# Optimization experiments

Measured on AMD Instinct MI355X. Metric: run time of the kernel, lower is better.

Reference implementation:

```python
import jax, jax.numpy as jnp
import numpy as np

B, S, D, H = 2, 2048, 1024, 16
HD = D // H  # head_dim = 64

def setup_inputs() -> dict:
    key = jax.random.key(0)
    ks = jax.random.split(key, 12)
    sc = 0.02
    return {
        "x": jax.random.normal(ks[0], (B, S, D), dtype=jnp.float32),
        "docking_scores": jax.random.uniform(ks[1], (B, S), dtype=jnp.float32),
        # weights stored as (in, out): y = x @ W + b (equivalent to torch Linear with W=weight.T)
        "Wq": jax.random.normal(ks[2], (D, D), dtype=jnp.float32) * sc,
        "bq": jnp.zeros((D,), dtype=jnp.float32),
        "Wk": jax.random.normal(ks[3], (D, D), dtype=jnp.float32) * sc,
        "bk": jnp.zeros((D,), dtype=jnp.float32),
        "Wv": jax.random.normal(ks[4], (D, D), dtype=jnp.float32) * sc,
        "bv": jnp.zeros((D,), dtype=jnp.float32),
        "Wo": jax.random.normal(ks[5], (D, D), dtype=jnp.float32) * sc,
        "bo": jnp.zeros((D,), dtype=jnp.float32),
        "beta": jnp.asarray(0.5, dtype=jnp.float32),
    }

def reference(x, docking_scores, Wq, bq, Wk, bk, Wv, bv, Wo, bo, beta):
    b, s, d = x.shape
    # project and split heads: (B, H, S, HD)
    def heads(y):
        return y.reshape(b, s, H, HD).transpose(0, 2, 1, 3)
    Q = heads(x @ Wq + bq)
    K = heads(x @ Wk + bk)
    V = heads(x @ Wv + bv)
    # full attention scores (B, H, S, S) — materialized as in the source
    scores = jnp.einsum('bhqd,bhkd->bhqk', Q, K) / np.float32(np.sqrt(HD))
    attn = jax.nn.softmax(scores, axis=-1)
    # docking blend: daa_type != ALL -> blend with per-key docking scores
    ds = docking_scores[:, None, None, :]  # (B, 1, 1, S)
    attn = (1.0 - beta) * attn + beta * ds
    ctx = jnp.einsum('bhqk,bhkd->bhqd', attn, V)
    ctx = ctx.transpose(0, 2, 1, 3).reshape(b, s, d)
    return ctx @ Wo + bo
```

## Files before the change

### kernel.cpp

```cpp
#include <hip/hip_runtime.h>

typedef __attribute__((ext_vector_type(8))) short short8;
typedef __attribute__((ext_vector_type(4))) short short4v;
typedef __attribute__((ext_vector_type(4))) float f32x4;

#if __has_builtin(__builtin_amdgcn_exp2f)
#define EXP2F(x) __builtin_amdgcn_exp2f(x)
#define QSCALE 0.1803368801111601f
#else
#define EXP2F(x) __expf(x)
#define QSCALE 0.125f
#endif

__device__ __forceinline__ short f2bf(float f) {
  unsigned u = __builtin_bit_cast(unsigned, f);
  u += 0x7fffu + ((u >> 16) & 1u);
  return (short)(u >> 16);
}
__device__ __forceinline__ float bf2f(short s) {
  unsigned u = ((unsigned)(unsigned short)s) << 16;
  return __builtin_bit_cast(float, u);
}
__device__ __forceinline__ void async_load16(const short* g, short* l) {
  __builtin_amdgcn_global_load_lds(
      (const __attribute__((address_space(1))) unsigned int*)g,
      (__attribute__((address_space(3))) unsigned int*)l, 16, 0, 0);
}

__global__ __launch_bounds__(256) void convert_x(const float* __restrict__ x,
                                                 short* __restrict__ xb) {
  int i = (blockIdx.x * 256 + threadIdx.x) * 4;
  float4 v = *(const float4*)(x + i);
  short4v o;
  o[0] = f2bf(v.x); o[1] = f2bf(v.y); o[2] = f2bf(v.z); o[3] = f2bf(v.w);
  *(short4v*)(xb + i) = o;
}

__global__ __launch_bounds__(256) void transpose_w(
    const float* __restrict__ W0, const float* __restrict__ W1,
    const float* __restrict__ W2, const float* __restrict__ W3,
    short* __restrict__ T0, short* __restrict__ T1,
    short* __restrict__ T2, short* __restrict__ T3) {
  const float* W; short* T;
  switch (blockIdx.z) {
    case 0: W = W0; T = T0; break;
    case 1: W = W1; T = T1; break;
    case 2: W = W2; T = T2; break;
    default: W = W3; T = T3; break;
  }
  __shared__ float tile[32][33];
  int tx = threadIdx.x & 31, ty = threadIdx.x >> 5;
  int c = blockIdx.x * 32 + tx;
  #pragma unroll
  for (int i = 0; i < 4; ++i) {
    int r = blockIdx.y * 32 + ty + i * 8;
    tile[ty + i * 8][tx] = W[(size_t)r * 1024 + c];
  }
  __syncthreads();
  int k = blockIdx.y * 32 + tx;
  #pragma unroll
  for (int i = 0; i < 4; ++i) {
    int n = blockIdx.x * 32 + ty + i * 8;
    T[(size_t)n * 1024 + k] = f2bf(tile[tx][ty + i * 8]);
  }
}

__device__ __forceinline__ void gemm_core_128(
    const short* __restrict__ A, const short* __restrict__ Bt,
    int m0, int n0, short* As, short* Bs, f32x4 acc[4][4]) {
  const int tid = threadIdx.x;
  const int wave = tid >> 6, lane = tid & 63;
  const int wm = wave >> 1, wn = wave & 1;
  const int lr = lane & 15, quad = lane >> 4;
  for (int k0 = 0; k0 < 1024; k0 += 32) {
    __syncthreads();
    #pragma unroll
    for (int c2 = 0; c2 < 2; ++c2) {
      int c = wave * 2 + c2;
      int row = c * 16 + (lane >> 2);
      int cbp = lane & 3;
      int sw = (cbp ^ ((row >> 1) & 3)) << 3;
      async_load16(A + (size_t)(m0 + row) * 1024 + k0 + sw, As + c * 512);
      async_load16(Bt + (size_t)(n0 + row) * 1024 + k0 + sw, Bs + c * 512);
    }
    __syncthreads();
    short8 af[4], bfr[4];
    #pragma unroll
    for (int i = 0; i < 4; ++i) {
      int ra = wm * 64 + i * 16 + lr;
      af[i] = *(const short8*)(As + ra * 32 + ((quad ^ ((ra >> 1) & 3)) << 3));
      int rb = wn * 64 + i * 16 + lr;
      bfr[i] = *(const short8*)(Bs + rb * 32 + ((quad ^ ((rb >> 1) & 3)) << 3));
    }
    #pragma unroll
    for (int i = 0; i < 4; ++i)
      #pragma unroll
      for (int j = 0; j < 4; ++j)
        acc[i][j] = __builtin_amdgcn_mfma_f32_16x16x32_bf16(af[i], bfr[j], acc[i][j], 0, 0, 0);
  }
}

__global__ __launch_bounds__(256, 2) void qkv_gemm(
    const short* __restrict__ xb,
    const short* __restrict__ WqT, const short* __restrict__ WkT, const short* __restrict__ WvT,
    const float* __restrict__ bq, const float* __restrict__ bk, const float* __restrict__ bv,
    short* __restrict__ Qb, short* __restrict__ Kb, short* __restrict__ Vt) {
  __shared__ short As[128 * 32];
  __shared__ short Bs[128 * 32];
  int which = blockIdx.x >> 3;
  int n0 = (blockIdx.x & 7) * 128;
  int m0 = blockIdx.y * 128;
  const short* Bt = (which == 0) ? WqT : (which == 1) ? WkT : WvT;
  const float* bias = (which == 0) ? bq : (which == 1) ? bk : bv;
  f32x4 acc[4][4] = {};
  gemm_core_128(xb, Bt, m0, n0, As, Bs, acc);
  const int lane = threadIdx.x & 63, wave = threadIdx.x >> 6;
  const int wm = wave >> 1, wn = wave & 1;
  const int lr = lane & 15, quad = lane >> 4;
  if (which < 2) {
    short* Out = (which == 0) ? Qb : Kb;
    const float scale = (which == 0) ? QSCALE : 1.0f;
    #pragma unroll
    for (int i = 0; i < 4; ++i)
      #pragma unroll
      for (int j = 0; j < 4; ++j) {
        int col = n0 + wn * 64 + j * 16 + lr;
        float bb = bias[col];
        int rowb = m0 + wm * 64 + i * 16 + quad * 4;
        #pragma unroll
        for (int r = 0; r < 4; ++r)
          Out[(size_t)(rowb + r) * 1024 + col] = f2bf((acc[i][j][r] + bb) * scale);
      }
  } else {
    #pragma unroll
    for (int i = 0; i < 4; ++i)
      #pragma unroll
      for (int j = 0; j < 4; ++j) {
        int col = n0 + wn * 64 + j * 16 + lr;
        float bb = bias[col];
        int h = col >> 6, d = col & 63;
        int rowb = m0 + wm * 64 + i * 16 + quad * 4;
        int b = rowb >> 11, s = rowb & 2047;
        short4v pk;
        #pragma unroll
        for (int r = 0; r < 4; ++r) pk[r] = f2bf(acc[i][j][r] + bb);
        *(short4v*)(Vt + ((size_t)(b * 16 + h) * 64 + d) * 2048 + s) = pk;
      }
  }
}

__global__ __launch_bounds__(256) void dsv_kernel(const short* __restrict__ Vt,
                                                  const float* __restrict__ ds,
                                                  float* __restrict__ dsV) {
  int bh = blockIdx.x, sc = blockIdx.y;
  int b = bh >> 4;
  int d = threadIdx.x >> 2, part = threadIdx.x & 3;
  const short* vrow = Vt + ((size_t)bh * 64 + d) * 2048 + sc * 256 + part * 64;
  const float* dsrow = ds + (size_t)b * 2048 + sc * 256 + part * 64;
  float acc = 0.f;
  #pragma unroll
  for (int i = 0; i < 64; i += 8) {
    short8 v = *(const short8*)(vrow + i);
    float4 f0 = *(const float4*)(dsrow + i);
    float4 f1 = *(const float4*)(dsrow + i + 4);
    acc += f0.x * bf2f(v[0]) + f0.y * bf2f(v[1]) + f0.z * bf2f(v[2]) + f0.w * bf2f(v[3]);
    acc += f1.x * bf2f(v[4]) + f1.y * bf2f(v[5]) + f1.z * bf2f(v[6]) + f1.w * bf2f(v[7]);
  }
  acc += __shfl_xor(acc, 1);
  acc += __shfl_xor(acc, 2);
  if (part == 0) atomicAdd(dsV + bh * 64 + d, acc);
}

__global__ __launch_bounds__(512, 4) void attn_kernel(
    const short* __restrict__ Qb, const short* __restrict__ Kb,
    const short* __restrict__ Vt, const float* __restrict__ dsV,
    const float* __restrict__ beta_p, short* __restrict__ ctx) {
  __shared__ short smem[32768];
  const int tid = threadIdx.x, wave = tid >> 6, lane = tid & 63;
  const int bh = blockIdx.x >> 4, qt = blockIdx.x & 15;
  const int b = bh >> 4, h = bh & 15;
  const size_t bS = (size_t)b * 2048;
  const int lr = lane & 15, quad = lane >> 4;
  const int half = wave >> 2;
  const int qg = wave & 3;
  const int q0 = qt * 128 + qg * 32;

  short* Ksh = smem + half * 8192;
  short* Vsh = Ksh + 4096;
  short* myP = smem + 16384 + wave * 2048;

  short8 qf[2][2];
  #pragma unroll
  for (int mb = 0; mb < 2; ++mb)
    #pragma unroll
    for (int c = 0; c < 2; ++c)
      qf[mb][c] = *(const short8*)(Qb + (bS + q0 + mb * 16 + lr) * 1024 + h * 64 + c * 32 + quad * 8);

  f32x4 O[2][4] = {};
  float lacc[2] = {0.f, 0.f};
  const int xs = (lr & 7) << 1;

  for (int t = 0; t < 16; ++t) {
    const int k0 = (half * 16 + t) * 64;
    __syncthreads();
    #pragma unroll
    for (int c4 = 0; c4 < 4; ++c4) {
      int c = qg * 4 + c4;
      int rloc = lane >> 3;
      int cbp = lane & 7;
      if (c < 8) {
        int rk = c * 8 + rloc;
        int sw = (cbp ^ (rk & 7)) << 3;
        async_load16(Kb + (bS + k0 + rk) * 1024 + h * 64 + sw, Ksh + c * 512);
      } else {
        int cv = c - 8;
        int rk = cv * 8 + rloc;
        int sw = (cbp ^ (rk & 7)) << 3;
        async_load16(Vt + ((size_t)bh * 64 + rk) * 2048 + k0 + sw, Vsh + cv * 512);
      }
    }
    __syncthreads();

    #pragma unroll
    for (int kb = 0; kb < 4; ++kb) {
      int krow = kb * 16 + lr;
      const short* kr = Ksh + krow * 64;
      short8 kf0 = *(const short8*)(kr + ((quad ^ (krow & 7)) << 3));
      short8 kf1 = *(const short8*)(kr + (((4 + quad) ^ (krow & 7)) << 3));
      #pragma unroll
      for (int mb = 0; mb < 2; ++mb) {
        f32x4 st = {0.f, 0.f, 0.f, 0.f};
        st = __builtin_amdgcn_mfma_f32_16x16x32_bf16(kf0, qf[mb][0], st, 0, 0, 0);
        st = __builtin_amdgcn_mfma_f32_16x16x32_bf16(kf1, qf[mb][1], st, 0, 0, 0);
        float p0 = EXP2F(st[0]), p1 = EXP2F(st[1]);
        float p2 = EXP2F(st[2]), p3 = EXP2F(st[3]);
        lacc[mb] += (p0 + p1) + (p2 + p3);
        unsigned a0 = __builtin_bit_cast(unsigned, p0) + 0x8000u;
        unsigned a1 = __builtin_bit_cast(unsigned, p1) + 0x8000u;
        unsigned a2 = __builtin_bit_cast(unsigned, p2) + 0x8000u;
        unsigned a3 = __builtin_bit_cast(unsigned, p3) + 0x8000u;
        uint2 pk;
        pk.x = (a0 >> 16) | (a1 & 0xffff0000u);
        pk.y = (a2 >> 16) | (a3 & 0xffff0000u);
        int qrl = mb * 16 + lr;
        int phys4 = (kb * 4 + quad) ^ xs;
        *(uint2*)(myP + qrl * 64 + (phys4 << 2)) = pk;
      }
    }
    #pragma unroll
    for (int kc = 0; kc < 2; ++kc) {
      short8 pf[2];
      #pragma unroll
      for (int mb = 0; mb < 2; ++mb) {
        int qrl = mb * 16 + lr;
        int phys = ((kc * 4 + quad) << 1) ^ xs;
        pf[mb] = *(const short8*)(myP + qrl * 64 + (phys << 2));
      }
      #pragma unroll
      for (int db = 0; db < 4; ++db) {
        int drow = db * 16 + lr;
        short8 vf = *(const short8*)(Vsh + drow * 64 + (((kc * 4 + quad) ^ (drow & 7)) << 3));
        #pragma unroll
        for (int mb = 0; mb < 2; ++mb)
          O[mb][db] = __builtin_amdgcn_mfma_f32_16x16x32_bf16(vf, pf[mb], O[mb][db], 0, 0, 0);
      }
    }
  }

  float* Obuf = (float*)smem;
  float* lbuf = (float*)(smem + 16384);
  __syncthreads();
  if (half == 1) {
    #pragma unroll
    for (int mb = 0; mb < 2; ++mb) {
      #pragma unroll
      for (int db = 0; db < 4; ++db)
        *(f32x4*)(Obuf + ((qg * 2 + mb) * 4 + db) * 256 + lr * 16 + quad * 4) = O[mb][db];
      lbuf[(qg * 2 + mb) * 64 + quad * 16 + lr] = lacc[mb];
    }
  }
  __syncthreads();
  if (half == 0) {
    #pragma unroll
    for (int mb = 0; mb < 2; ++mb) {
      #pragma unroll
      for (int db = 0; db < 4; ++db)
        O[mb][db] += *(const f32x4*)(Obuf + ((qg * 2 + mb) * 4 + db) * 256 + lr * 16 + quad * 4);
      lacc[mb] += lbuf[(qg * 2 + mb) * 64 + quad * 16 + lr];
      float v = lacc[mb];
      v += __shfl_xor(v, 16);
      v += __shfl_xor(v, 32);
      lacc[mb] = v;
    }
    float beta = *beta_p;
    #pragma unroll
    for (int mb = 0; mb < 2; ++mb) {
      float linv = (1.f - beta) / lacc[mb];
      #pragma unroll
      for (int db = 0; db < 4; ++db) {
        float4 dv = *(const float4*)(dsV + bh * 64 + db * 16 + quad * 4);
        short4v o;
        o[0] = f2bf(O[mb][db][0] * linv + beta * dv.x);
        o[1] = f2bf(O[mb][db][1] * linv + beta * dv.y);
        o[2] = f2bf(O[mb][db][2] * linv + beta * dv.z);
        o[3] = f2bf(O[mb][db][3] * linv + beta * dv.w);
        *(short4v*)(ctx + (bS + q0 + mb * 16 + lr) * 1024 + h * 64 + db * 16 + quad * 4) = o;
      }
    }
  }
}

__global__ __launch_bounds__(256, 2) void out_gemm(
    const short* __restrict__ ctx, const short* __restrict__ WoT,
    const float* __restrict__ bo, float* __restrict__ out) {
  __shared__ short As[64 * 32];
  __shared__ short Bs[128 * 32];
  const int n0 = blockIdx.x * 128, m0 = blockIdx.y * 64;
  const int tid = threadIdx.x, wave = tid >> 6, lane = tid & 63;
  const int wm = wave >> 1, wn = wave & 1;
  const int lr = lane & 15, quad = lane >> 4;
  f32x4 acc[2][4] = {};
  for (int k0 = 0; k0 < 1024; k0 += 32) {
    __syncthreads();
    #pragma unroll
    for (int c3 = 0; c3 < 3; ++c3) {
      int idx = wave * 3 + c3;
      int rloc = lane >> 2;
      int cbp = lane & 3;
      if (idx < 4) {
        int row = idx * 16 + rloc;
        int sw = (cbp ^ ((row >> 1) & 3)) << 3;
        async_load16(ctx + (size_t)(m0 + row) * 1024 + k0 + sw, As + idx * 512);
      } else {
        int c = idx - 4;
        int row = c * 16 + rloc;
        int sw = (cbp ^ ((row >> 1) & 3)) << 3;
        async_load16(WoT + (size_t)(n0 + row) * 1024 + k0 + sw, Bs + c * 512);
      }
    }
    __syncthreads();
    short8 af[2], bfr[4];
    #pragma unroll
    for (int i = 0; i < 2; ++i) {
      int ra = wm * 32 + i * 16 + lr;
      af[i] = *(const short8*)(As + ra * 32 + ((quad ^ ((ra >> 1) & 3)) << 3));
    }
    #pragma unroll
    for (int j = 0; j < 4; ++j) {
      int rb = wn * 64 + j * 16 + lr;
      bfr[j] = *(const short8*)(Bs + rb * 32 + ((quad ^ ((rb >> 1) & 3)) << 3));
    }
    #pragma unroll
    for (int i = 0; i < 2; ++i)
      #pragma unroll
      for (int j = 0; j < 4; ++j)
        acc[i][j] = __builtin_amdgcn_mfma_f32_16x16x32_bf16(af[i], bfr[j], acc[i][j], 0, 0, 0);
  }
  #pragma unroll
  for (int i = 0; i < 2; ++i)
    #pragma unroll
    for (int j = 0; j < 4; ++j) {
      int col = n0 + wn * 64 + j * 16 + lr;
      float bb = bo[col];
      int rowb = m0 + wm * 32 + i * 16 + quad * 4;
      #pragma unroll
      for (int r = 0; r < 4; ++r)
        out[(size_t)(rowb + r) * 1024 + col] = acc[i][j][r] + bb;
    }
}

extern "C" void kernel_launch(void* const* d_in, const int* in_sizes, int n_in,
                              void* d_out, int out_size, void* d_ws, size_t ws_size,
                              hipStream_t stream) {
  const float* x    = (const float*)d_in[0];
  const float* dsc  = (const float*)d_in[1];
  const float* Wq   = (const float*)d_in[2];
  const float* bq   = (const float*)d_in[3];
  const float* Wk   = (const float*)d_in[4];
  const float* bk   = (const float*)d_in[5];
  const float* Wv   = (const float*)d_in[6];
  const float* bv   = (const float*)d_in[7];
  const float* Wo   = (const float*)d_in[8];
  const float* bo   = (const float*)d_in[9];
  const float* beta = (const float*)d_in[10];

  char* ws = (char*)d_ws;
  const size_t MB = 1u << 20;
  short* xb  = (short*)(ws + 0 * MB);
  short* WqT = (short*)(ws + 8 * MB);
  short* WkT = (short*)(ws + 10 * MB);
  short* WvT = (short*)(ws + 12 * MB);
  short* WoT = (short*)(ws + 14 * MB);
  short* Qb  = (short*)(ws + 16 * MB);
  short* Kb  = (short*)(ws + 24 * MB);
  short* Vt  = (short*)(ws + 32 * MB);
  float* dsV = (float*)(ws + 40 * MB);
  short* ctx = xb;

  convert_x<<<4096, 256, 0, stream>>>(x, xb);
  transpose_w<<<dim3(32, 32, 4), 256, 0, stream>>>(Wq, Wk, Wv, Wo, WqT, WkT, WvT, WoT);
  qkv_gemm<<<dim3(24, 32), 256, 0, stream>>>(xb, WqT, WkT, WvT, bq, bk, bv, Qb, Kb, Vt);
  hipMemsetAsync(dsV, 0, 32 * 64 * sizeof(float), stream);
  dsv_kernel<<<dim3(32, 8), 256, 0, stream>>>(Vt, dsc, dsV);
  attn_kernel<<<512, 512, 0, stream>>>(Qb, Kb, Vt, dsV, beta, ctx);
  out_gemm<<<dim3(8, 64), 256, 0, stream>>>(ctx, WoT, bo, (float*)d_out);
}
```

Before: 213.0 us.

## Halve attention block waves, give each wave 64 query rows for K/V reuse

The attention kernel now launches 256 threads (4 waves) per block instead of 512, and each wave handles 64 query rows (4 MFMA row blocks) instead of 32. Each K/V fragment read from LDS therefore feeds twice as many MFMAs. The loader is split so one wave group loads K and the other loads V. Bf16 packing now uses v_perm, and the final reduction buffer uses a rotated column index to reduce bank conflicts. The cost is more registers per wave (accumulators double) and less latency hiding from fewer waves per block.

```diff
diff --git a/kernel.cpp b/kernel.cpp
--- a/kernel.cpp
+++ b/kernel.cpp
@@ -171,7 +171,7 @@
   if (part == 0) atomicAdd(dsV + bh * 64 + d, acc);
 }
 
-__global__ __launch_bounds__(512, 4) void attn_kernel(
+__global__ __launch_bounds__(256, 2) void attn_kernel(
     const short* __restrict__ Qb, const short* __restrict__ Kb,
     const short* __restrict__ Vt, const float* __restrict__ dsV,
     const float* __restrict__ beta_p, short* __restrict__ ctx) {
@@ -181,54 +181,53 @@
   const int b = bh >> 4, h = bh & 15;
   const size_t bS = (size_t)b * 2048;
   const int lr = lane & 15, quad = lane >> 4;
-  const int half = wave >> 2;
-  const int qg = wave & 3;
-  const int q0 = qt * 128 + qg * 32;
+  const int qg = wave & 1, half = wave >> 1;
+  const int q0 = qt * 128 + qg * 64;
+  const int lm7 = lane & 7;
+  const int l7 = lr & 7;
 
   short* Ksh = smem + half * 8192;
   short* Vsh = Ksh + 4096;
-  short* myP = smem + 16384 + wave * 2048;
-
-  short8 qf[2][2];
+  short* myP = smem + 16384 + wave * 4096;
+
+  short8 qf[4][2];
   #pragma unroll
-  for (int mb = 0; mb < 2; ++mb)
+  for (int mb = 0; mb < 4; ++mb)
     #pragma unroll
     for (int c = 0; c < 2; ++c)
       qf[mb][c] = *(const short8*)(Qb + (bS + q0 + mb * 16 + lr) * 1024 + h * 64 + c * 32 + quad * 8);
 
-  f32x4 O[2][4] = {};
-  float lacc[2] = {0.f, 0.f};
-  const int xs = (lr & 7) << 1;
+  f32x4 O[4][4] = {};
+  float lacc[4] = {0.f, 0.f, 0.f, 0.f};
+
+  const int srow = lane >> 3;
+  const int scb = (lane & 7) ^ srow;
 
   for (int t = 0; t < 16; ++t) {
     const int k0 = (half * 16 + t) * 64;
     __syncthreads();
-    #pragma unroll
-    for (int c4 = 0; c4 < 4; ++c4) {
-      int c = qg * 4 + c4;
-      int rloc = lane >> 3;
-      int cbp = lane & 7;
-      if (c < 8) {
-        int rk = c * 8 + rloc;
-        int sw = (cbp ^ (rk & 7)) << 3;
-        async_load16(Kb + (bS + k0 + rk) * 1024 + h * 64 + sw, Ksh + c * 512);
-      } else {
-        int cv = c - 8;
-        int rk = cv * 8 + rloc;
-        int sw = (cbp ^ (rk & 7)) << 3;
-        async_load16(Vt + ((size_t)bh * 64 + rk) * 2048 + k0 + sw, Vsh + cv * 512);
+    if (qg == 0) {
+      #pragma unroll
+      for (int c = 0; c < 8; ++c) {
+        int rk = c * 8 + srow;
+        async_load16(Kb + (bS + k0 + rk) * 1024 + h * 64 + scb * 8, Ksh + c * 512);
+      }
+    } else {
+      #pragma unroll
+      for (int c = 0; c < 8; ++c) {
+        int rv = c * 8 + srow;
+        async_load16(Vt + ((size_t)bh * 64 + rv) * 2048 + k0 + scb * 8, Vsh + c * 512);
       }
     }
     __syncthreads();
 
     #pragma unroll
     for (int kb = 0; kb < 4; ++kb) {
-      int krow = kb * 16 + lr;
-      const short* kr = Ksh + krow * 64;
-      short8 kf0 = *(const short8*)(kr + ((quad ^ (krow & 7)) << 3));
-      short8 kf1 = *(const short8*)(kr + (((4 + quad) ^ (krow & 7)) << 3));
-      #pragma unroll
-      for (int mb = 0; mb < 2; ++mb) {
+      const short* kr = Ksh + (kb * 16 + lr) * 64;
+      short8 kf0 = *(const short8*)(kr + ((quad ^ l7) << 3));
+      short8 kf1 = *(const short8*)(kr + (((4 + quad) ^ l7) << 3));
+      #pragma unroll
+      for (int mb = 0; mb < 4; ++mb) {
         f32x4 st = {0.f, 0.f, 0.f, 0.f};
         st = __builtin_amdgcn_mfma_f32_16x16x32_bf16(kf0, qf[mb][0], st, 0, 0, 0);
         st = __builtin_amdgcn_mfma_f32_16x16x32_bf16(kf1, qf[mb][1], st, 0, 0, 0);
@@ -240,28 +239,26 @@
         unsigned a2 = __builtin_bit_cast(unsigned, p2) + 0x8000u;
         unsigned a3 = __builtin_bit_cast(unsigned, p3) + 0x8000u;
         uint2 pk;
-        pk.x = (a0 >> 16) | (a1 & 0xffff0000u);
-        pk.y = (a2 >> 16) | (a3 & 0xffff0000u);
-        int qrl = mb * 16 + lr;
-        int phys4 = (kb * 4 + quad) ^ xs;
-        *(uint2*)(myP + qrl * 64 + (phys4 << 2)) = pk;
+        pk.x = __builtin_amdgcn_perm(a1, a0, 0x07060302u);
+        pk.y = __builtin_amdgcn_perm(a3, a2, 0x07060302u);
+        int phys = (4 * kb + quad) ^ (2 * l7);
+        *(uint2*)(myP + (mb * 16 + lr) * 64 + phys * 4) = pk;
       }
     }
     #pragma unroll
     for (int kc = 0; kc < 2; ++kc) {
-      short8 pf[2];
-      #pragma unroll
-      for (int mb = 0; mb < 2; ++mb) {
-        int qrl = mb * 16 + lr;
-        int phys = ((kc * 4 + quad) << 1) ^ xs;
-        pf[mb] = *(const short8*)(myP + qrl * 64 + (phys << 2));
+      short8 pf[4];
+      #pragma unroll
+      for (int mb = 0; mb < 4; ++mb) {
+        int phys = (8 * kc + 2 * quad) ^ (2 * l7);
+        pf[mb] = *(const short8*)(myP + (mb * 16 + lr) * 64 + phys * 4);
       }
       #pragma unroll
       for (int db = 0; db < 4; ++db) {
-        int drow = db * 16 + lr;
-        short8 vf = *(const short8*)(Vsh + drow * 64 + (((kc * 4 + quad) ^ (drow & 7)) << 3));
+        const short* vr = Vsh + (db * 16 + lr) * 64;
+        short8 vf = *(const short8*)(vr + (((kc * 4 + quad) ^ l7) << 3));
         #pragma unroll
-        for (int mb = 0; mb < 2; ++mb)
+        for (int mb = 0; mb < 4; ++mb)
           O[mb][db] = __builtin_amdgcn_mfma_f32_16x16x32_bf16(vf, pf[mb], O[mb][db], 0, 0, 0);
       }
     }
@@ -269,33 +266,29 @@
 
   float* Obuf = (float*)smem;
   float* lbuf = (float*)(smem + 16384);
+  const int qs = (quad + lr) & 3;
   __syncthreads();
   if (half == 1) {
     #pragma unroll
-    for (int mb = 0; mb < 2; ++mb) {
+    for (int mb = 0; mb < 4; ++mb) {
       #pragma unroll
       for (int db = 0; db < 4; ++db)
-        *(f32x4*)(Obuf + ((qg * 2 + mb) * 4 + db) * 256 + lr * 16 + quad * 4) = O[mb][db];
-      lbuf[(qg * 2 + mb) * 64 + quad * 16 + lr] = lacc[mb];
+        *(f32x4*)(Obuf + ((qg * 4 + mb) * 4 + db) * 256 + lr * 16 + qs * 4) = O[mb][db];
+      lbuf[(qg * 4 + mb) * 64 + quad * 16 + lr] = lacc[mb];
     }
   }
   __syncthreads();
   if (half == 0) {
-    #pragma unroll
-    for (int mb = 0; mb < 2; ++mb) {
+    float beta = *beta_p;
+    #pragma unroll
+    for (int mb = 0; mb < 4; ++mb) {
       #pragma unroll
       for (int db = 0; db < 4; ++db)
-        O[mb][db] += *(const f32x4*)(Obuf + ((qg * 2 + mb) * 4 + db) * 256 + lr * 16 + quad * 4);
-      lacc[mb] += lbuf[(qg * 2 + mb) * 64 + quad * 16 + lr];
-      float v = lacc[mb];
+        O[mb][db] += *(const f32x4*)(Obuf + ((qg * 4 + mb) * 4 + db) * 256 + lr * 16 + qs * 4);
+      float v = lacc[mb] + lbuf[(qg * 4 + mb) * 64 + quad * 16 + lr];
       v += __shfl_xor(v, 16);
       v += __shfl_xor(v, 32);
-      lacc[mb] = v;
-    }
-    float beta = *beta_p;
-    #pragma unroll
-    for (int mb = 0; mb < 2; ++mb) {
-      float linv = (1.f - beta) / lacc[mb];
+      float linv = (1.f - beta) / v;
       #pragma unroll
       for (int db = 0; db < 4; ++db) {
         float4 dv = *(const float4*)(dsV + bh * 64 + db * 16 + quad * 4);
@@ -402,6 +395,6 @@
   qkv_gemm<<<dim3(24, 32), 256, 0, stream>>>(xb, WqT, WkT, WvT, bq, bk, bv, Qb, Kb, Vt);
   hipMemsetAsync(dsV, 0, 32 * 64 * sizeof(float), stream);
   dsv_kernel<<<dim3(32, 8), 256, 0, stream>>>(Vt, dsc, dsV);
-  attn_kernel<<<512, 512, 0, stream>>>(Qb, Kb, Vt, dsV, beta, ctx);
+  attn_kernel<<<512, 256, 0, stream>>>(Qb, Kb, Vt, dsV, beta, ctx);
   out_gemm<<<dim3(8, 64), 256, 0, stream>>>(ctx, WoT, bo, (float*)d_out);
 }
```

Measured after the change: 205.4 us (median of 2 runs). 3.6% less time.
